# Kernel tuning notes

Measured on AMD Instinct MI355X. Metric: run time of the kernel, lower is better.

The kernel has to match this reference:

```python
import jax, jax.numpy as jnp
import numpy as np

NEG_SLOPE = 0.2

def _gat_attn(inp, W, a_src, a_dst):
    # inp: [G, N, C]; W: [H, C]; a_src/a_dst: [H, 1]
    x = jnp.einsum('gnc,hc->gnh', inp, W)          # Linear (no bias)
    x = jnp.where(x >= 0, x, NEG_SLOPE * x)         # LeakyReLU(0.2)
    s = jnp.einsum('gnh,ho->gn', x, a_src)          # [G, N]
    d = jnp.einsum('gnh,ho->gn', x, a_dst)          # [G, N]
    e = s[:, :, None] + d[:, None, :]               # e[g,i,j] = s_i + d_j
    return jax.nn.softmax(e, axis=-1)               # [G, N, N]

def setup_inputs() -> dict:
    key = jax.random.key(0)
    ks = jax.random.split(key, 9)
    B, C, T, J, H = 4096, 128, 10, 22, 128
    return {
        'src':     jax.random.normal(ks[0], (B, C, T, J), dtype=jnp.float32),
        'W_s':     jax.random.normal(ks[1], (H, C), dtype=jnp.float32) * 0.1,
        'a_src_s': jax.random.normal(ks[2], (H, 1), dtype=jnp.float32) * 0.1,
        'a_dst_s': jax.random.normal(ks[3], (H, 1), dtype=jnp.float32) * 0.1,
        'W_t':     jax.random.normal(ks[4], (H, C), dtype=jnp.float32) * 0.1,
        'a_src_t': jax.random.normal(ks[5], (H, 1), dtype=jnp.float32) * 0.1,
        'a_dst_t': jax.random.normal(ks[6], (H, 1), dtype=jnp.float32) * 0.1,
        'sa_bias': jax.random.normal(ks[7], (1, J, J), dtype=jnp.float32) * 0.1,
        'ta_bias': jax.random.normal(ks[8], (1, T, T), dtype=jnp.float32) * 0.1,
    }

def reference(src, W_s, a_src_s, a_dst_s, W_t, a_src_t, a_dst_t, sa_bias, ta_bias):
    B, C, T, J = src.shape
    # spatial branch: [B*T, J, C]
    sp = jnp.transpose(src, (0, 2, 3, 1)).reshape(B * T, J, C)
    sa = _gat_attn(sp, W_s, a_src_s, a_dst_s)                 # [B*T, J, J]
    # temporal branch: [B*J, T, C]
    tp = jnp.transpose(src, (0, 3, 2, 1)).reshape(B * J, T, C)
    ta = _gat_attn(tp, W_t, a_src_t, a_dst_t)                 # [B*J, T, T]
    sa_fusion = sa.reshape(B, T, J, J) + sa_bias[None]        # broadcast bias
    ta_fusion = ta.reshape(B, J, T, T) + ta_bias[None]
    zero = jnp.float32(0.0)
    return (sa_fusion, ta_fusion, zero, zero, zero, zero)
```

## Files before the change

kernel.cpp:

```cpp
#include <hip/hip_runtime.h>
#include <math.h>

#define NB 4096
#define CC 128
#define TT 10
#define JJ 22
#define MM 220
#define WSTRIDE 68
#define OUT0_N 19824640
#define OUT1_N 9011200

typedef __attribute__((ext_vector_type(8))) short bf16x8;
typedef __attribute__((ext_vector_type(4))) float f32x4;

__device__ __forceinline__ unsigned f2bf(float f) {
  union { float f; unsigned u; } v; v.f = f;
  return (v.u + 0x7FFFu + ((v.u >> 16) & 1u)) >> 16;
}

__global__ __launch_bounds__(448, 4) void dms_fused(
    const float* __restrict__ src,
    const float* __restrict__ Ws,
    const float* __restrict__ a_dst_s,
    const float* __restrict__ Wt,
    const float* __restrict__ a_dst_t,
    const float* __restrict__ sa_bias,
    const float* __restrict__ ta_bias,
    float* __restrict__ out)
{
  __shared__ unsigned lds_w[256 * WSTRIDE];
  __shared__ float a_l[256];
  __shared__ float ds_l[MM];
  __shared__ float dt_l[MM];

  const int tid  = threadIdx.x;
  const int w    = tid >> 6;
  const int lane = tid & 63;
  const int l15  = lane & 15;
  const int quad = lane >> 4;
  const int b    = blockIdx.x;

  const float* srcb = src + (size_t)b * (CC * MM);

  bf16x8 Aa[2][4];
  #pragma unroll
  for (int mtp = 0; mtp < 2; ++mtp) {
    int m = (w * 2 + mtp) * 16 + l15;
    if (m > MM - 1) m = MM - 1;
    #pragma unroll
    for (int kf = 0; kf < 4; ++kf) {
      const float* p = srcb + (kf * 32 + quad * 8) * MM + m;
      bf16x8 f;
      #pragma unroll
      for (int j = 0; j < 8; ++j)
        f[j] = (short)f2bf(p[j * MM]);
      Aa[mtp][kf] = f;
    }
  }

  for (int p4 = tid; p4 < 256 * 64; p4 += 448) {
    int n = p4 >> 6, kw = p4 & 63;
    const float* wp = (n < 128) ? (Ws + n * CC + kw * 2)
                                : (Wt + (n - 128) * CC + kw * 2);
    lds_w[n * WSTRIDE + kw] = f2bf(wp[0]) | (f2bf(wp[1]) << 16);
  }
  if (tid < 256)
    a_l[tid] = (tid < 128) ? a_dst_s[tid] : a_dst_t[tid - 128];
  __syncthreads();

  f32x4 part_s0 = {0,0,0,0}, part_s1 = {0,0,0,0};
  f32x4 part_t0 = {0,0,0,0}, part_t1 = {0,0,0,0};
  const unsigned short* wl = (const unsigned short*)lds_w;
  #pragma unroll
  for (int nt = 0; nt < 16; ++nt) {
    const bf16x8* bp = (const bf16x8*)(wl + (nt * 16 + l15) * (WSTRIDE * 2) + quad * 8);
    f32x4 acc0 = {0,0,0,0}, acc1 = {0,0,0,0};
    #pragma unroll
    for (int kf = 0; kf < 4; ++kf) {
      bf16x8 bb = bp[kf * 4];
      acc0 = __builtin_amdgcn_mfma_f32_16x16x32_bf16(Aa[0][kf], bb, acc0, 0, 0, 0);
      acc1 = __builtin_amdgcn_mfma_f32_16x16x32_bf16(Aa[1][kf], bb, acc1, 0, 0, 0);
    }
    float av = a_l[nt * 16 + l15];
    #pragma unroll
    for (int r = 0; r < 4; ++r) {
      float x0 = acc0[r]; x0 = (x0 >= 0.f) ? x0 : 0.2f * x0;
      float x1 = acc1[r]; x1 = (x1 >= 0.f) ? x1 : 0.2f * x1;
      if (nt < 8) { part_s0[r] += av * x0; part_s1[r] += av * x1; }
      else        { part_t0[r] += av * x0; part_t1[r] += av * x1; }
    }
  }

  #pragma unroll
  for (int mk = 1; mk <= 8; mk <<= 1) {
    #pragma unroll
    for (int r = 0; r < 4; ++r) {
      part_s0[r] += __shfl_xor(part_s0[r], mk);
      part_s1[r] += __shfl_xor(part_s1[r], mk);
      part_t0[r] += __shfl_xor(part_t0[r], mk);
      part_t1[r] += __shfl_xor(part_t1[r], mk);
    }
  }
  if (l15 == 0) {
    #pragma unroll
    for (int r = 0; r < 4; ++r) {
      int m0 = (w * 2) * 16 + quad * 4 + r;
      if (m0 < MM) { ds_l[m0] = part_s0[r]; dt_l[m0] = part_t0[r]; }
      int m1 = (w * 2 + 1) * 16 + quad * 4 + r;
      if (m1 < MM) { ds_l[m1] = part_s1[r]; dt_l[m1] = part_t1[r]; }
    }
  }
  __syncthreads();

  for (int t = w; t < TT; t += 7) {
    float e = (lane < JJ) ? ds_l[t * JJ + lane] : -1e30f;
    float mx = e;
    #pragma unroll
    for (int mk = 1; mk < 64; mk <<= 1) mx = fmaxf(mx, __shfl_xor(mx, mk));
    float pp = (lane < JJ) ? __expf(e - mx) : 0.f;
    float ss = pp;
    #pragma unroll
    for (int mk = 1; mk < 64; mk <<= 1) ss += __shfl_xor(ss, mk);
    pp = pp / ss;
    float* o = out + (size_t)(b * TT + t) * (JJ * JJ);
    #pragma unroll
    for (int base = 0; base < 484; base += 64) {
      int oi = base + lane;
      int jdx = oi % JJ;
      float v = __shfl(pp, jdx);
      if (oi < 484) o[oi] = v + sa_bias[oi];
    }
  }

  float* out1 = out + (size_t)OUT0_N;
  for (int jdx = w; jdx < JJ; jdx += 7) {
    float e = (lane < TT) ? dt_l[lane * JJ + jdx] : -1e30f;
    float mx = e;
    #pragma unroll
    for (int mk = 1; mk < 64; mk <<= 1) mx = fmaxf(mx, __shfl_xor(mx, mk));
    float qq = (lane < TT) ? __expf(e - mx) : 0.f;
    float ss = qq;
    #pragma unroll
    for (int mk = 1; mk < 64; mk <<= 1) ss += __shfl_xor(ss, mk);
    qq = qq / ss;
    float* o = out1 + (size_t)(b * JJ + jdx) * (TT * TT);
    #pragma unroll
    for (int base = 0; base < 128; base += 64) {
      int oi = base + lane;
      int tdx = oi % TT;
      float v = __shfl(qq, tdx);
      if (oi < 100) o[oi] = v + ta_bias[oi];
    }
  }

  if (b == 0 && tid < 4) out[(size_t)OUT0_N + OUT1_N + tid] = 0.f;
}

extern "C" void kernel_launch(void* const* d_in, const int* in_sizes, int n_in,
                              void* d_out, int out_size, void* d_ws, size_t ws_size,
                              hipStream_t stream) {
  const float* src = (const float*)d_in[0];
  const float* Ws  = (const float*)d_in[1];
  const float* ads = (const float*)d_in[3];
  const float* Wt  = (const float*)d_in[4];
  const float* adt = (const float*)d_in[6];
  const float* sab = (const float*)d_in[7];
  const float* tab = (const float*)d_in[8];
  dms_fused<<<NB, 448, 0, stream>>>(src, Ws, ads, Wt, adt, sab, tab, (float*)d_out);
}
```

Baseline: 738.7 us.

## Split into persistent GEMM kernel with prefetch and separate vectorized softmax epilogue

Splits the fused kernel into two launches. The GEMM kernel processes 8 batches per block, which amortizes the bf16 weight staging into LDS, and prefetches the next batch's inputs into registers while the current batch's MFMAs run. The dst scores go to workspace and are read back by a second kernel that does the softmax with bias cached in LDS and float4 stores. This cuts the repeated weight loading per batch, at the cost of an extra launch, a workspace round trip, and fewer blocks (512) in the GEMM grid.

Measured after the change: 884.4 us. 19.7% more time.

```diff
diff --git a/kernel.cpp b/kernel.cpp
--- a/kernel.cpp
+++ b/kernel.cpp
@@ -9,6 +9,7 @@
 #define WSTRIDE 68
 #define OUT0_N 19824640
 #define OUT1_N 9011200
+#define BPB 8
 
 typedef __attribute__((ext_vector_type(8))) short bf16x8;
 typedef __attribute__((ext_vector_type(4))) float f32x4;
@@ -18,45 +19,40 @@
   return (v.u + 0x7FFFu + ((v.u >> 16) & 1u)) >> 16;
 }
 
-__global__ __launch_bounds__(448, 4) void dms_fused(
+__device__ __forceinline__ void load_A(bf16x8 A[2][4], const float* __restrict__ srcb,
+                                       int w, int l15, int quad) {
+  #pragma unroll
+  for (int mtp = 0; mtp < 2; ++mtp) {
+    int m = w * 32 + mtp * 16 + l15;
+    if (m > MM - 1) m = MM - 1;
+    #pragma unroll
+    for (int kf = 0; kf < 4; ++kf) {
+      const float* p = srcb + (kf * 32 + quad * 8) * MM + m;
+      bf16x8 f;
+      #pragma unroll
+      for (int j = 0; j < 8; ++j)
+        f[j] = (short)f2bf(p[j * MM]);
+      A[mtp][kf] = f;
+    }
+  }
+}
+
+__global__ __launch_bounds__(448) void dms_gemm(
     const float* __restrict__ src,
     const float* __restrict__ Ws,
     const float* __restrict__ a_dst_s,
     const float* __restrict__ Wt,
     const float* __restrict__ a_dst_t,
-    const float* __restrict__ sa_bias,
-    const float* __restrict__ ta_bias,
-    float* __restrict__ out)
+    float* __restrict__ dws)
 {
   __shared__ unsigned lds_w[256 * WSTRIDE];
   __shared__ float a_l[256];
-  __shared__ float ds_l[MM];
-  __shared__ float dt_l[MM];
 
   const int tid  = threadIdx.x;
   const int w    = tid >> 6;
   const int lane = tid & 63;
   const int l15  = lane & 15;
   const int quad = lane >> 4;
-  const int b    = blockIdx.x;
-
-  const float* srcb = src + (size_t)b * (CC * MM);
-
-  bf16x8 Aa[2][4];
-  #pragma unroll
-  for (int mtp = 0; mtp < 2; ++mtp) {
-    int m = (w * 2 + mtp) * 16 + l15;
-    if (m > MM - 1) m = MM - 1;
-    #pragma unroll
-    for (int kf = 0; kf < 4; ++kf) {
-      const float* p = srcb + (kf * 32 + quad * 8) * MM + m;
-      bf16x8 f;
-      #pragma unroll
-      for (int j = 0; j < 8; ++j)
-        f[j] = (short)f2bf(p[j * MM]);
-      Aa[mtp][kf] = f;
-    }
-  }
 
   for (int p4 = tid; p4 < 256 * 64; p4 += 448) {
     int n = p4 >> 6, kw = p4 & 63;
@@ -68,51 +64,97 @@
     a_l[tid] = (tid < 128) ? a_dst_s[tid] : a_dst_t[tid - 128];
   __syncthreads();
 
-  f32x4 part_s0 = {0,0,0,0}, part_s1 = {0,0,0,0};
-  f32x4 part_t0 = {0,0,0,0}, part_t1 = {0,0,0,0};
   const unsigned short* wl = (const unsigned short*)lds_w;
-  #pragma unroll
-  for (int nt = 0; nt < 16; ++nt) {
-    const bf16x8* bp = (const bf16x8*)(wl + (nt * 16 + l15) * (WSTRIDE * 2) + quad * 8);
-    f32x4 acc0 = {0,0,0,0}, acc1 = {0,0,0,0};
-    #pragma unroll
-    for (int kf = 0; kf < 4; ++kf) {
-      bf16x8 bb = bp[kf * 4];
-      acc0 = __builtin_amdgcn_mfma_f32_16x16x32_bf16(Aa[0][kf], bb, acc0, 0, 0, 0);
-      acc1 = __builtin_amdgcn_mfma_f32_16x16x32_bf16(Aa[1][kf], bb, acc1, 0, 0, 0);
-    }
-    float av = a_l[nt * 16 + l15];
-    #pragma unroll
-    for (int r = 0; r < 4; ++r) {
-      float x0 = acc0[r]; x0 = (x0 >= 0.f) ? x0 : 0.2f * x0;
-      float x1 = acc1[r]; x1 = (x1 >= 0.f) ? x1 : 0.2f * x1;
-      if (nt < 8) { part_s0[r] += av * x0; part_s1[r] += av * x1; }
-      else        { part_t0[r] += av * x0; part_t1[r] += av * x1; }
-    }
-  }
-
-  #pragma unroll
-  for (int mk = 1; mk <= 8; mk <<= 1) {
-    #pragma unroll
-    for (int r = 0; r < 4; ++r) {
-      part_s0[r] += __shfl_xor(part_s0[r], mk);
-      part_s1[r] += __shfl_xor(part_s1[r], mk);
-      part_t0[r] += __shfl_xor(part_t0[r], mk);
-      part_t1[r] += __shfl_xor(part_t1[r], mk);
-    }
-  }
-  if (l15 == 0) {
-    #pragma unroll
-    for (int r = 0; r < 4; ++r) {
-      int m0 = (w * 2) * 16 + quad * 4 + r;
-      if (m0 < MM) { ds_l[m0] = part_s0[r]; dt_l[m0] = part_t0[r]; }
-      int m1 = (w * 2 + 1) * 16 + quad * 4 + r;
-      if (m1 < MM) { ds_l[m1] = part_s1[r]; dt_l[m1] = part_t1[r]; }
-    }
-  }
+  const int b0 = blockIdx.x * BPB;
+
+  bf16x8 Acur[2][4];
+  load_A(Acur, src + (size_t)b0 * (CC * MM), w, l15, quad);
+
+  for (int ib = 0; ib < BPB; ++ib) {
+    const int b = b0 + ib;
+
+    bf16x8 Anext[2][4];
+    if (ib < BPB - 1)
+      load_A(Anext, src + (size_t)(b + 1) * (CC * MM), w, l15, quad);
+
+    f32x4 part_s0 = {0,0,0,0}, part_s1 = {0,0,0,0};
+    f32x4 part_t0 = {0,0,0,0}, part_t1 = {0,0,0,0};
+    #pragma unroll
+    for (int nt = 0; nt < 16; ++nt) {
+      const bf16x8* bp = (const bf16x8*)(wl + (nt * 16 + l15) * (WSTRIDE * 2) + quad * 8);
+      f32x4 acc0 = {0,0,0,0}, acc1 = {0,0,0,0};
+      #pragma unroll
+      for (int kf = 0; kf < 4; ++kf) {
+        bf16x8 bb = bp[kf * 4];
+        acc0 = __builtin_amdgcn_mfma_f32_16x16x32_bf16(Acur[0][kf], bb, acc0, 0, 0, 0);
+        acc1 = __builtin_amdgcn_mfma_f32_16x16x32_bf16(Acur[1][kf], bb, acc1, 0, 0, 0);
+      }
+      float av = a_l[nt * 16 + l15];
+      #pragma unroll
+      for (int r = 0; r < 4; ++r) {
+        float x0 = fmaxf(acc0[r], 0.2f * acc0[r]);
+        float x1 = fmaxf(acc1[r], 0.2f * acc1[r]);
+        if (nt < 8) { part_s0[r] += av * x0; part_s1[r] += av * x1; }
+        else        { part_t0[r] += av * x0; part_t1[r] += av * x1; }
+      }
+    }
+
+    #pragma unroll
+    for (int mk = 1; mk <= 8; mk <<= 1) {
+      #pragma unroll
+      for (int r = 0; r < 4; ++r) {
+        part_s0[r] += __shfl_xor(part_s0[r], mk);
+        part_s1[r] += __shfl_xor(part_s1[r], mk);
+        part_t0[r] += __shfl_xor(part_t0[r], mk);
+        part_t1[r] += __shfl_xor(part_t1[r], mk);
+      }
+    }
+    if (l15 == 0) {
+      float* dsb = dws + (size_t)b * MM;
+      float* dtb = dws + (size_t)NB * MM + (size_t)b * MM;
+      #pragma unroll
+      for (int r = 0; r < 4; ++r) {
+        int m0 = w * 32 + quad * 4 + r;
+        if (m0 < MM) { dsb[m0] = part_s0[r]; dtb[m0] = part_t0[r]; }
+        int m1 = w * 32 + 16 + quad * 4 + r;
+        if (m1 < MM) { dsb[m1] = part_s1[r]; dtb[m1] = part_t1[r]; }
+      }
+    }
+
+    if (ib < BPB - 1) {
+      #pragma unroll
+      for (int mtp = 0; mtp < 2; ++mtp)
+        #pragma unroll
+        for (int kf = 0; kf < 4; ++kf)
+          Acur[mtp][kf] = Anext[mtp][kf];
+    }
+  }
+}
+
+__global__ __launch_bounds__(256) void dms_epilogue(
+    const float* __restrict__ dws,
+    const float* __restrict__ sa_bias,
+    const float* __restrict__ ta_bias,
+    float* __restrict__ out)
+{
+  __shared__ __align__(16) float ds_l[MM];
+  __shared__ __align__(16) float dt_l[MM];
+  __shared__ __align__(16) float sab_l[484];
+  __shared__ __align__(16) float tab_l[100];
+
+  const int tid  = threadIdx.x;
+  const int w    = tid >> 6;
+  const int lane = tid & 63;
+  const int b    = blockIdx.x;
+
+  const float* dsp = dws + (size_t)b * MM;
+  const float* dtp = dws + (size_t)NB * MM + (size_t)b * MM;
+  for (int i = tid; i < MM; i += 256) { ds_l[i] = dsp[i]; dt_l[i] = dtp[i]; }
+  for (int i = tid; i < 484; i += 256) sab_l[i] = sa_bias[i];
+  if (tid < 100) tab_l[tid] = ta_bias[tid];
   __syncthreads();
 
-  for (int t = w; t < TT; t += 7) {
+  for (int t = w; t < TT; t += 4) {
     float e = (lane < JJ) ? ds_l[t * JJ + lane] : -1e30f;
     float mx = e;
     #pragma unroll
@@ -122,19 +164,22 @@
     #pragma unroll
     for (int mk = 1; mk < 64; mk <<= 1) ss += __shfl_xor(ss, mk);
     pp = pp / ss;
-    float* o = out + (size_t)(b * TT + t) * (JJ * JJ);
-    #pragma unroll
-    for (int base = 0; base < 484; base += 64) {
-      int oi = base + lane;
-      int jdx = oi % JJ;
-      float v = __shfl(pp, jdx);
-      if (oi < 484) o[oi] = v + sa_bias[oi];
+    float4* o = (float4*)(out + (size_t)(b * TT + t) * 484);
+    const float4* bias4 = (const float4*)sab_l;
+    for (int f = lane; f < 121; f += 64) {
+      float4 bv = bias4[f];
+      float4 v;
+      v.x = __shfl(pp, (4 * f + 0) % JJ) + bv.x;
+      v.y = __shfl(pp, (4 * f + 1) % JJ) + bv.y;
+      v.z = __shfl(pp, (4 * f + 2) % JJ) + bv.z;
+      v.w = __shfl(pp, (4 * f + 3) % JJ) + bv.w;
+      o[f] = v;
     }
   }
 
   float* out1 = out + (size_t)OUT0_N;
-  for (int jdx = w; jdx < JJ; jdx += 7) {
-    float e = (lane < TT) ? dt_l[lane * JJ + jdx] : -1e30f;
+  for (int j = w; j < JJ; j += 4) {
+    float e = (lane < TT) ? dt_l[lane * JJ + j] : -1e30f;
     float mx = e;
     #pragma unroll
     for (int mk = 1; mk < 64; mk <<= 1) mx = fmaxf(mx, __shfl_xor(mx, mk));
@@ -143,14 +188,15 @@
     #pragma unroll
     for (int mk = 1; mk < 64; mk <<= 1) ss += __shfl_xor(ss, mk);
     qq = qq / ss;
-    float* o = out1 + (size_t)(b * JJ + jdx) * (TT * TT);
-    #pragma unroll
-    for (int base = 0; base < 128; base += 64) {
-      int oi = base + lane;
-      int tdx = oi % TT;
-      float v = __shfl(qq, tdx);
-      if (oi < 100) o[oi] = v + ta_bias[oi];
-    }
+    float4* o = (float4*)(out1 + (size_t)(b * JJ + j) * 100);
+    const float4* bias4 = (const float4*)tab_l;
+    float4 v;
+    float4 bv = (lane < 25) ? bias4[lane] : make_float4(0, 0, 0, 0);
+    v.x = __shfl(qq, (4 * lane + 0) % TT) + bv.x;
+    v.y = __shfl(qq, (4 * lane + 1) % TT) + bv.y;
+    v.z = __shfl(qq, (4 * lane + 2) % TT) + bv.z;
+    v.w = __shfl(qq, (4 * lane + 3) % TT) + bv.w;
+    if (lane < 25) o[lane] = v;
   }
 
   if (b == 0 && tid < 4) out[(size_t)OUT0_N + OUT1_N + tid] = 0.f;
@@ -166,5 +212,8 @@
   const float* adt = (const float*)d_in[6];
   const float* sab = (const float*)d_in[7];
   const float* tab = (const float*)d_in[8];
-  dms_fused<<<NB, 448, 0, stream>>>(src, Ws, ads, Wt, adt, sab, tab, (float*)d_out);
-}
+  float* dws = (float*)d_ws;
+
+  dms_gemm<<<NB / BPB, 448, 0, stream>>>(src, Ws, ads, Wt, adt, dws);
+  dms_epilogue<<<NB, 256, 0, stream>>>(dws, sab, tab, (float*)d_out);
+}
```
